# Kernel optimization log

Measured on AMD Instinct MI355X. Metric: run time of the kernel, lower is better.

## Reference

```python
import jax, jax.numpy as jnp
import numpy as np

EPS = 1e-08
SURROGATE_SCALE = 10.0  # SuperSpike surrogate slope

@jax.custom_vjp
def spike_fn(v):
    # Heaviside forward, SuperSpike surrogate gradient backward
    return (v > 0).astype(v.dtype)

def _spike_fwd(v):
    return spike_fn(v), v

def _spike_bwd(v, g):
    return (g / (1.0 + SURROGATE_SCALE * jnp.abs(v)) ** 2,)

spike_fn.defvjp(_spike_fwd, _spike_bwd)


def setup_inputs() -> dict:
    key = jax.random.key(0)
    k1, k2, k3, k4 = jax.random.split(key, 4)
    B, C, T = 64, 256, 2048
    x = jax.random.normal(k1, (B, C, T), dtype=jnp.float32)
    conv_weight = jax.random.normal(k2, (C, C, 3), dtype=jnp.float32) * 0.05
    beta = jnp.clip(0.7 + 0.01 * jax.random.normal(k3, (1,), dtype=jnp.float32), 0.0, 1.0)
    b = jnp.clip(1.0 + 0.01 * jax.random.normal(k4, (C,), dtype=jnp.float32), 0.0, None)
    return {"x": x, "conv_weight": conv_weight, "beta": beta, "b": b}


def reference(x, conv_weight, beta, b):
    # x: (B, C, T); LIF recurrence over T with scaled threshold/reset
    norm = (conv_weight ** 2).sum((1, 2))          # (C,)
    inv_norm = 1.0 / (norm + EPS)                   # (C,)
    B, C, T = x.shape
    xt = jnp.transpose(x, (2, 0, 1))                # (T, B, C)

    def step(carry, inp):
        mem, spk = carry
        rst = spk * (b * norm)                      # einsum ab,b,b->ab
        mem = (mem - rst) * beta + inp * (1.0 - beta)
        mthr = mem * inv_norm - b
        spk = spike_fn(mthr)
        return (mem, spk), spk

    init = (jnp.zeros((B, C), x.dtype), jnp.zeros((B, C), x.dtype))
    _, spk_rec = jax.lax.scan(step, init, xt)       # (T, B, C)
    return jnp.transpose(spk_rec, (1, 2, 0))        # (B, C, T), flatten_output=False
```

## Files before the change

kernel.cpp:

```cpp
#include <hip/hip_runtime.h>

#define C_DIM 256
#define T_DIM 2048
#define B_DIM 64
#define NROWS (B_DIM * C_DIM)
#define SEGS 8
#define SEGL (T_DIM / SEGS)
#define WARM 128
#define CV 8
#define WCH (WARM / (CV * 4))
#define MCH (SEGL / (CV * 4))

__device__ __forceinline__ float sqrn(float v) { return __fmul_rn(v, v); }

__global__ __launch_bounds__(64) void norm_kernel(const float* __restrict__ w,
                                                  const float* __restrict__ b,
                                                  float* __restrict__ bn,
                                                  float* __restrict__ ninv) {
    const int c = blockIdx.x;
    const int k = threadIdx.x;
    __shared__ float q[8];
    if (k < 8) {
        const float* a = w + c * 768 + k * 96;
        float r0 = sqrn(a[0]), r1 = sqrn(a[1]), r2 = sqrn(a[2]), r3 = sqrn(a[3]);
        float r4 = sqrn(a[4]), r5 = sqrn(a[5]), r6 = sqrn(a[6]), r7 = sqrn(a[7]);
        #pragma unroll
        for (int i = 8; i < 96; i += 8) {
            r0 = __fadd_rn(r0, sqrn(a[i + 0]));
            r1 = __fadd_rn(r1, sqrn(a[i + 1]));
            r2 = __fadd_rn(r2, sqrn(a[i + 2]));
            r3 = __fadd_rn(r3, sqrn(a[i + 3]));
            r4 = __fadd_rn(r4, sqrn(a[i + 4]));
            r5 = __fadd_rn(r5, sqrn(a[i + 5]));
            r6 = __fadd_rn(r6, sqrn(a[i + 6]));
            r7 = __fadd_rn(r7, sqrn(a[i + 7]));
        }
        q[k] = __fadd_rn(__fadd_rn(__fadd_rn(r0, r1), __fadd_rn(r2, r3)),
                         __fadd_rn(__fadd_rn(r4, r5), __fadd_rn(r6, r7)));
    }
    __syncthreads();
    if (k == 0) {
        float s = __fadd_rn(__fadd_rn(__fadd_rn(q[0], q[1]), __fadd_rn(q[2], q[3])),
                            __fadd_rn(__fadd_rn(q[4], q[5]), __fadd_rn(q[6], q[7])));
        bn[c]   = __fmul_rn(b[c], s);
        ninv[c] = 1.0f / __fadd_rn(s, 1e-8f);
    }
}

__device__ __forceinline__ float step_fast(float xw, float& mem, int& mask,
                                           float bnc, float beta, float nic, float bc) {
    float m0 = __fmul_rn(mem, beta);
    float m1 = __fmul_rn(__fsub_rn(mem, bnc), beta);
    m0 = __fadd_rn(m0, xw);
    m1 = __fadd_rn(m1, xw);
    int mi = (__float_as_int(m1) & mask) | (__float_as_int(m0) & ~mask);
    mem = __int_as_float(mi);
    float p = __fmul_rn(mem, nic);
    float d = __fsub_rn(bc, p);
    mask = __float_as_int(d) >> 31;
    return __int_as_float(mask & 0x3f800000);
}

#define STEP4_NOSTORE(v)                                                   \
    do {                                                                   \
        float xw0 = __fmul_rn((v).x, omb);                                 \
        float xw1 = __fmul_rn((v).y, omb);                                 \
        float xw2 = __fmul_rn((v).z, omb);                                 \
        float xw3 = __fmul_rn((v).w, omb);                                 \
        (void)step_fast(xw0, mem, mask, bnc, beta, nic, bc);               \
        (void)step_fast(xw1, mem, mask, bnc, beta, nic, bc);               \
        (void)step_fast(xw2, mem, mask, bnc, beta, nic, bc);               \
        (void)step_fast(xw3, mem, mask, bnc, beta, nic, bc);               \
    } while (0)

#define STEP4_STORE(v, o)                                                  \
    do {                                                                   \
        float xw0 = __fmul_rn((v).x, omb);                                 \
        float xw1 = __fmul_rn((v).y, omb);                                 \
        float xw2 = __fmul_rn((v).z, omb);                                 \
        float xw3 = __fmul_rn((v).w, omb);                                 \
        (o).x = step_fast(xw0, mem, mask, bnc, beta, nic, bc);             \
        (o).y = step_fast(xw1, mem, mask, bnc, beta, nic, bc);             \
        (o).z = step_fast(xw2, mem, mask, bnc, beta, nic, bc);             \
        (o).w = step_fast(xw3, mem, mask, bnc, beta, nic, bc);             \
    } while (0)

__global__ __launch_bounds__(256, 2) void lif_seg_kernel(const float* __restrict__ x,
                                                         const float* __restrict__ beta_p,
                                                         const float* __restrict__ b,
                                                         const float* __restrict__ bn,
                                                         const float* __restrict__ ninv,
                                                         float* __restrict__ out) {
    const int tid = blockIdx.x * 256 + threadIdx.x;
    const int seg = tid & (SEGS - 1);
    const int row = tid >> 3;
    const int c   = row & (C_DIM - 1);

    const float beta = beta_p[0];
    const float omb  = __fsub_rn(1.0f, beta);
    const float bnc  = bn[c];
    const float nic  = ninv[c];
    const float bc   = b[c];

    const float* xs = x + (size_t)row * T_DIM + seg * SEGL;

    float mem = 0.0f;
    int   mask = 0;

    if (seg != 0) {
        const float4* wp = (const float4*)(xs - WARM);
        float4 A[CV], Bb[CV];
        #pragma unroll
        for (int i = 0; i < CV; ++i) A[i] = wp[i];
        #pragma unroll 1
        for (int ch = 0; ch < WCH; ch += 2) {
            #pragma unroll
            for (int i = 0; i < CV; ++i) Bb[i] = wp[(ch + 1) * CV + i];
            #pragma unroll
            for (int i = 0; i < CV; ++i) STEP4_NOSTORE(A[i]);
            if (ch + 2 < WCH) {
                #pragma unroll
                for (int i = 0; i < CV; ++i) A[i] = wp[(ch + 2) * CV + i];
            }
            #pragma unroll
            for (int i = 0; i < CV; ++i) STEP4_NOSTORE(Bb[i]);
        }
    }

    const float4* mp = (const float4*)xs;
    float4*       op = (float4*)(out + (size_t)row * T_DIM + seg * SEGL);

    float4 A[CV], Bb[CV];
    #pragma unroll
    for (int i = 0; i < CV; ++i) A[i] = mp[i];
    #pragma unroll 1
    for (int ch = 0; ch < MCH; ch += 2) {
        #pragma unroll
        for (int i = 0; i < CV; ++i) Bb[i] = mp[(ch + 1) * CV + i];
        #pragma unroll
        for (int i = 0; i < CV; ++i) {
            float4 o;
            STEP4_STORE(A[i], o);
            op[ch * CV + i] = o;
        }
        if (ch + 2 < MCH) {
            #pragma unroll
            for (int i = 0; i < CV; ++i) A[i] = mp[(ch + 2) * CV + i];
        }
        #pragma unroll
        for (int i = 0; i < CV; ++i) {
            float4 o;
            STEP4_STORE(Bb[i], o);
            op[(ch + 1) * CV + i] = o;
        }
    }
}

extern "C" void kernel_launch(void* const* d_in, const int* in_sizes, int n_in,
                              void* d_out, int out_size, void* d_ws, size_t ws_size,
                              hipStream_t stream) {
    const float* x    = (const float*)d_in[0];
    const float* w    = (const float*)d_in[1];
    const float* beta = (const float*)d_in[2];
    const float* b    = (const float*)d_in[3];
    float* out  = (float*)d_out;
    float* bn   = (float*)d_ws;
    float* ninv = bn + C_DIM;

    norm_kernel<<<C_DIM, 64, 0, stream>>>(w, b, bn, ninv);
    lif_seg_kernel<<<(NROWS * SEGS) / 256, 256, 0, stream>>>(x, beta, b, bn, ninv, out);
}
```

Before: 300.3 us.

## Stage LIF segment loads and stores through LDS for coalesced access

Reworks the LIF kernel into single-wavefront blocks. Each block stages 64-step phases of its 64 segment streams through padded shared memory, so global loads and stores are coalesced across lanes instead of each thread walking its own strided row. Warm-up and main phases are merged into one phase loop, and segment 0 resets its state after the warm-up. It relies on a single wave with lgkmcnt waits instead of barriers, and it loses the register-level double-buffered prefetch, so load latency is exposed at each phase.

Result: faster. 252.9 us (-15.8%).

```diff
diff --git a/kernel.cpp b/kernel.cpp
--- a/kernel.cpp
+++ b/kernel.cpp
@@ -7,9 +7,11 @@
 #define SEGS 8
 #define SEGL (T_DIM / SEGS)
 #define WARM 128
-#define CV 8
-#define WCH (WARM / (CV * 4))
-#define MCH (SEGL / (CV * 4))
+#define PW   64
+#define NPH  ((WARM + SEGL) / PW)
+#define WARM_PH (WARM / PW)
+#define SPITCH 68
+#define NSTR 64
 
 __device__ __forceinline__ float sqrn(float v) { return __fmul_rn(v, v); }
 
@@ -85,16 +87,20 @@
         (o).w = step_fast(xw3, mem, mask, bnc, beta, nic, bc);             \
     } while (0)
 
-__global__ __launch_bounds__(256, 2) void lif_seg_kernel(const float* __restrict__ x,
-                                                         const float* __restrict__ beta_p,
-                                                         const float* __restrict__ b,
-                                                         const float* __restrict__ bn,
-                                                         const float* __restrict__ ninv,
-                                                         float* __restrict__ out) {
-    const int tid = blockIdx.x * 256 + threadIdx.x;
-    const int seg = tid & (SEGS - 1);
-    const int row = tid >> 3;
-    const int c   = row & (C_DIM - 1);
+#define WAITCNT_LGKM0  0xC07F
+
+__global__ __launch_bounds__(64) void lif_seg_kernel(const float* __restrict__ x,
+                                                     const float* __restrict__ beta_p,
+                                                     const float* __restrict__ b,
+                                                     const float* __restrict__ bn,
+                                                     const float* __restrict__ ninv,
+                                                     float* __restrict__ out) {
+    __shared__ __align__(16) float lds[NSTR * SPITCH];
+
+    const int lane = threadIdx.x;
+    const int seg  = lane & 7;
+    const int row  = blockIdx.x * 8 + (lane >> 3);
+    const int c    = row & (C_DIM - 1);
 
     const float beta = beta_p[0];
     const float omb  = __fsub_rn(1.0f, beta);
@@ -102,56 +108,55 @@
     const float nic  = ninv[c];
     const float bc   = b[c];
 
-    const float* xs = x + (size_t)row * T_DIM + seg * SEGL;
+    const int fh = lane >> 4;
+    const int fj = lane & 15;
 
     float mem = 0.0f;
     int   mask = 0;
 
-    if (seg != 0) {
-        const float4* wp = (const float4*)(xs - WARM);
-        float4 A[CV], Bb[CV];
+    float* my = &lds[lane * SPITCH];
+
+    #pragma unroll 1
+    for (int P = 0; P < NPH; ++P) {
         #pragma unroll
-        for (int i = 0; i < CV; ++i) A[i] = wp[i];
-        #pragma unroll 1
-        for (int ch = 0; ch < WCH; ch += 2) {
+        for (int q = 0; q < 16; ++q) {
+            const int s    = 4 * q + fh;
+            const int srow = blockIdx.x * 8 + (s >> 3);
+            int rel = (s & 7) * SEGL - WARM + P * PW;
+            if (rel < 0) rel = 0;
+            const float* g = x + (size_t)srow * T_DIM + rel + 4 * fj;
+            float4 v = *(const float4*)g;
+            *(float4*)(&lds[s * SPITCH + 4 * fj]) = v;
+        }
+        __builtin_amdgcn_s_waitcnt(WAITCNT_LGKM0);
+
+        if (P < WARM_PH) {
             #pragma unroll
-            for (int i = 0; i < CV; ++i) Bb[i] = wp[(ch + 1) * CV + i];
+            for (int g = 0; g < PW / 4; ++g) {
+                float4 v = *(const float4*)(my + 4 * g);
+                STEP4_NOSTORE(v);
+            }
+            if (P == WARM_PH - 1) {
+                if (seg == 0) { mem = 0.0f; mask = 0; }
+            }
+        } else {
             #pragma unroll
-            for (int i = 0; i < CV; ++i) STEP4_NOSTORE(A[i]);
-            if (ch + 2 < WCH) {
-                #pragma unroll
-                for (int i = 0; i < CV; ++i) A[i] = wp[(ch + 2) * CV + i];
+            for (int g = 0; g < PW / 4; ++g) {
+                float4 v = *(const float4*)(my + 4 * g);
+                float4 o;
+                STEP4_STORE(v, o);
+                *(float4*)(my + 4 * g) = o;
             }
+            __builtin_amdgcn_s_waitcnt(WAITCNT_LGKM0);
+
             #pragma unroll
-            for (int i = 0; i < CV; ++i) STEP4_NOSTORE(Bb[i]);
-        }
-    }
-
-    const float4* mp = (const float4*)xs;
-    float4*       op = (float4*)(out + (size_t)row * T_DIM + seg * SEGL);
-
-    float4 A[CV], Bb[CV];
-    #pragma unroll
-    for (int i = 0; i < CV; ++i) A[i] = mp[i];
-    #pragma unroll 1
-    for (int ch = 0; ch < MCH; ch += 2) {
-        #pragma unroll
-        for (int i = 0; i < CV; ++i) Bb[i] = mp[(ch + 1) * CV + i];
-        #pragma unroll
-        for (int i = 0; i < CV; ++i) {
-            float4 o;
-            STEP4_STORE(A[i], o);
-            op[ch * CV + i] = o;
-        }
-        if (ch + 2 < MCH) {
-            #pragma unroll
-            for (int i = 0; i < CV; ++i) A[i] = mp[(ch + 2) * CV + i];
-        }
-        #pragma unroll
-        for (int i = 0; i < CV; ++i) {
-            float4 o;
-            STEP4_STORE(Bb[i], o);
-            op[(ch + 1) * CV + i] = o;
+            for (int q = 0; q < 16; ++q) {
+                const int s    = 4 * q + fh;
+                const int srow = blockIdx.x * 8 + (s >> 3);
+                const int rel  = (s & 7) * SEGL - WARM + P * PW;
+                float4 v = *(const float4*)(&lds[s * SPITCH + 4 * fj]);
+                *(float4*)(out + (size_t)srow * T_DIM + rel + 4 * fj) = v;
+            }
         }
     }
 }
@@ -168,5 +173,5 @@
     float* ninv = bn + C_DIM;
 
     norm_kernel<<<C_DIM, 64, 0, stream>>>(w, b, bn, ninv);
-    lif_seg_kernel<<<(NROWS * SEGS) / 256, 256, 0, stream>>>(x, beta, b, bn, ninv, out);
+    lif_seg_kernel<<<(NROWS * SEGS) / NSTR, NSTR, 0, stream>>>(x, beta, b, bn, ninv, out);
 }
```
